# Kernel tuning notes

Measured on AMD Instinct MI355X. Metric: run time of the kernel, lower is better.

Reference implementation:

```python
import jax, jax.numpy as jnp
import numpy as np

N = 100000      # nodes
E = 3200000     # edges
G = 128         # graphs in batch
D_IN = 128
D_H = 256
D_OUT = 64
BN_EPS = 1e-3


def setup_inputs() -> dict:
    key = jax.random.key(0)
    ks = jax.random.split(key, 12)
    h = jax.random.normal(ks[0], (N, D_IN), jnp.float32)
    src = jax.random.randint(ks[1], (E,), 0, N, jnp.int32)
    dst = jax.random.randint(ks[2], (E,), 0, N, jnp.int32)
    graph_ids = jnp.sort(jax.random.randint(ks[3], (N,), 0, G, jnp.int32))
    # GraphConv weights (DGL default: weight + bias)
    W0 = jax.random.normal(ks[4], (D_IN, D_H), jnp.float32) * 0.05
    b0 = jnp.zeros((D_H,), jnp.float32)
    W = jax.random.normal(ks[5], (2, D_H, D_H), jnp.float32) * 0.05  # layers 1,2
    b = jnp.zeros((2, D_H), jnp.float32)
    # BatchNorm1d params (eval mode: running stats), 3 norm layers
    bn_gamma = jnp.ones((3, D_H), jnp.float32)
    bn_beta = jnp.zeros((3, D_H), jnp.float32)
    bn_mean = jax.random.normal(ks[6], (3, D_H), jnp.float32) * 0.1
    bn_var = jax.random.uniform(ks[7], (3, D_H), jnp.float32, 0.5, 1.5)
    # prediction head
    Wp = jax.random.normal(ks[8], (D_H, D_OUT), jnp.float32) * 0.05
    bp = jnp.zeros((D_OUT,), jnp.float32)
    return {"h": h, "W0": W0, "b0": b0, "W": W, "b": b,
            "bn_gamma": bn_gamma, "bn_beta": bn_beta, "bn_mean": bn_mean,
            "bn_var": bn_var, "Wp": Wp, "bp": bp,
            "src": src, "dst": dst, "graph_ids": graph_ids}


def reference(h, W0, b0, W, b, bn_gamma, bn_beta, bn_mean, bn_var, Wp, bp,
              src, dst, graph_ids):
    n = h.shape[0]
    ones_e = jnp.ones(src.shape, h.dtype)
    # symmetric normalization (DGL GraphConv norm='both'), degrees clamped to 1
    out_deg = jax.ops.segment_sum(ones_e, src, num_segments=n)
    in_deg = jax.ops.segment_sum(ones_e, dst, num_segments=n)
    norm_src = jax.lax.rsqrt(jnp.clip(out_deg, 1.0))  # [N]
    norm_dst = jax.lax.rsqrt(jnp.clip(in_deg, 1.0))   # [N]

    def graph_conv(x, Wl, bl):
        x = (x * norm_src[:, None]) @ Wl              # transform first (mult W then aggregate)
        agg = jax.ops.segment_sum(x[src], dst, num_segments=n)  # SpMM: gather+scatter-add
        return agg * norm_dst[:, None] + bl

    Ws = [W0, W[0], W[1]]
    bs = [b0, b[0], b[1]]
    for i in range(3):
        x = h
        h = graph_conv(h, Ws[i], bs[i])
        # BatchNorm1d in eval mode (running stats), eps=1e-3
        h = (h - bn_mean[i]) * jax.lax.rsqrt(bn_var[i] + BN_EPS) * bn_gamma[i] + bn_beta[i]
        h = jax.nn.relu(h) + (x if i != 0 else 0.0)   # residual skipped on first layer

    # mean pooling per graph
    counts = jax.ops.segment_sum(jnp.ones((n,), h.dtype), graph_ids, num_segments=G)
    pooled = jax.ops.segment_sum(h, graph_ids, num_segments=G) / jnp.clip(counts, 1.0)[:, None]
    return pooled @ Wp + bp
```

## Files before the change

### kernel.cpp

```cpp
#include <hip/hip_runtime.h>
#include <hip/hip_bf16.h>

#define NN 100000
#define EE 3200000
#define GG 128
#define D_IN 128
#define D_H 256
#define D_OUT 64
#define BN_EPS 1e-3f
#define PAD 96
#define LDSTRIDE 40
#define X8SCALE 16.0f
#define X8INV   0.0625f

#define NBUCK 782
#define BUCKET_CAP 5120
#define EPT 32

#define GEMM_NWG 6252

typedef __hip_bfloat16 bf16;
typedef __attribute__((ext_vector_type(8))) short short8;
typedef __attribute__((ext_vector_type(4))) float float4v;
typedef __attribute__((ext_vector_type(2))) float float2v;
typedef __attribute__((ext_vector_type(4))) int intv4;
typedef __attribute__((ext_vector_type(4))) unsigned short usv4;

#if __has_builtin(__builtin_amdgcn_cvt_pk_f32_fp8) && __has_builtin(__builtin_amdgcn_cvt_pk_fp8_f32)
#define HAVE_FP8_CVT 1
#endif

__device__ inline float bfbits2f(unsigned short s) {
    union { unsigned int u; float f; } c; c.u = ((unsigned int)s) << 16; return c.f;
}
__device__ inline unsigned short f2bfbits(float f) {
    union { float f; unsigned int u; } c; c.f = f;
    unsigned int r = c.u + 0x7fffu + ((c.u >> 16) & 1u);
    return (unsigned short)(r >> 16);
}
__device__ inline float4 load4us(const unsigned short* p) {
    ushort4 u = *(const ushort4*)p;
    return make_float4(bfbits2f(u.x), bfbits2f(u.y), bfbits2f(u.z), bfbits2f(u.w));
}
__device__ inline void store4us(unsigned short* p, float4 v) {
    ushort4 u;
    u.x = f2bfbits(v.x); u.y = f2bfbits(v.y); u.z = f2bfbits(v.z); u.w = f2bfbits(v.w);
    *(ushort4*)p = u;
}
__device__ inline float4 load4us_nt(const unsigned short* p) {
    usv4 u = __builtin_nontemporal_load((const usv4*)p);
    return make_float4(bfbits2f(u.x), bfbits2f(u.y), bfbits2f(u.z), bfbits2f(u.w));
}

__device__ inline unsigned char enc_fp8(float f) {
#ifdef HAVE_FP8_CVT
    int r = __builtin_amdgcn_cvt_pk_fp8_f32(f, f, 0, false);
    return (unsigned char)(r & 0xFF);
#else
    union { float f; unsigned u; } c; c.f = f;
    unsigned s = (c.u >> 31) << 7;
    float a = fabsf(f);
    if (!(a >= 0.015625f)) {
        int q = (int)rintf(a * 512.0f);
        return (unsigned char)(s | (unsigned)q);
    }
    if (a >= 464.0f) return (unsigned char)(s | 0x7E);
    int e = (int)((c.u >> 23) & 0xFF) - 127;
    int q = (int)rintf(ldexpf(a, 3 - e));
    if (q == 16) { q = 8; e += 1; }
    return (unsigned char)(s | ((unsigned)(e + 7) << 3) | (unsigned)(q - 8));
#endif
}
__device__ inline unsigned int enc4_fp8(float4 v) {
#ifdef HAVE_FP8_CVT
    int r = __builtin_amdgcn_cvt_pk_fp8_f32(v.x, v.y, 0, false);
    r = __builtin_amdgcn_cvt_pk_fp8_f32(v.z, v.w, r, true);
    return (unsigned int)r;
#else
    return (unsigned int)enc_fp8(v.x) | ((unsigned int)enc_fp8(v.y) << 8)
         | ((unsigned int)enc_fp8(v.z) << 16) | ((unsigned int)enc_fp8(v.w) << 24);
#endif
}
__device__ inline float4 dec4_fp8(unsigned int w) {
#ifdef HAVE_FP8_CVT
    float2v lo = __builtin_amdgcn_cvt_pk_f32_fp8((int)w, false);
    float2v hi = __builtin_amdgcn_cvt_pk_f32_fp8((int)w, true);
    return make_float4(lo.x, lo.y, hi.x, hi.y);
#else
    float4 o;
    unsigned b0 = w & 0xFF, b1 = (w >> 8) & 0xFF, b2 = (w >> 16) & 0xFF, b3 = w >> 24;
    auto d1 = [](unsigned b) -> float {
        unsigned s = b >> 7, e = (b >> 3) & 0xF, m = b & 7;
        float v = e ? ldexpf((float)(8 + m), (int)e - 10) : ldexpf((float)m, -9);
        return s ? -v : v;
    };
    o.x = d1(b0); o.y = d1(b1); o.z = d1(b2); o.w = d1(b3);
    return o;
#endif
}

__device__ inline int xcd_swz_gemm(int bid) {
    int x = bid & 7, i = bid >> 3;
    return (x < 4 ? x * 782 : 3128 + (x - 4) * 781) + i;
}

__global__ __launch_bounds__(1024) void k_bucket(const int* __restrict__ src,
                                                 const int* __restrict__ dst,
                                                 int* __restrict__ cursor,
                                                 int* __restrict__ scursor,
                                                 int* __restrict__ ebuf,
                                                 unsigned char* __restrict__ sbuf, int e) {
    __shared__ int hist[NBUCK];
    __shared__ int base[NBUCK];
    __shared__ int shist[NBUCK];
    __shared__ int sbase[NBUCK];
    int t = threadIdx.x;
    for (int i = t; i < NBUCK; i += 1024) { hist[i] = 0; shist[i] = 0; }
    __syncthreads();
    int e0 = blockIdx.x * (1024 * EPT) + t;
    int vals[EPT]; int bks[EPT];
#pragma unroll
    for (int j = 0; j < EPT; ++j) {
        int idx = e0 + j * 1024;
        bks[j] = -1;
        if (idx < e) {
            int s = src[idx], d = dst[idx];
            bks[j] = d >> 7;
            vals[j] = (s << 7) | (d & 127);
            atomicAdd(&hist[bks[j]], 1);
            atomicAdd(&shist[s >> 7], 1);
        }
    }
    __syncthreads();
    for (int i = t; i < NBUCK; i += 1024) {
        int c = hist[i];
        base[i] = c ? atomicAdd(&cursor[i], c) : 0;
        hist[i] = 0;
        int sc = shist[i];
        sbase[i] = sc ? atomicAdd(&scursor[i], sc) : 0;
        shist[i] = 0;
    }
    __syncthreads();
#pragma unroll
    for (int j = 0; j < EPT; ++j) {
        if (bks[j] >= 0) {
            int v = vals[j];
            int rel = base[bks[j]] + atomicAdd(&hist[bks[j]], 1);
            if (rel < BUCKET_CAP) ebuf[bks[j] * BUCKET_CAP + rel] = v;
            int sbk = v >> 14;
            int srel = sbase[sbk] + atomicAdd(&shist[sbk], 1);
            if (srel < BUCKET_CAP) sbuf[(size_t)sbk * BUCKET_CAP + srel] = (unsigned char)((v >> 7) & 127);
        }
    }
}

__global__ __launch_bounds__(256) void k_fill(const int* __restrict__ cursor,
                                              const int* __restrict__ scursor,
                                              const int* __restrict__ ebuf,
                                              const unsigned char* __restrict__ sbuf,
                                              int* __restrict__ col_pad,
                                              int* __restrict__ deg_in,
                                              float* __restrict__ norm_src,
                                              float* __restrict__ norm_dst) {
    __shared__ int lcol[128 * PAD];
    __shared__ int ldeg[128];
    __shared__ int lodeg[128];
    int b = blockIdx.x;
    int t = threadIdx.x;
    if (t < 128) { ldeg[t] = 0; lodeg[t] = 0; }
    __syncthreads();
    int cnt = cursor[b]; if (cnt > BUCKET_CAP) cnt = BUCKET_CAP;
    const int* eb = ebuf + b * BUCKET_CAP;
    for (int i = t; i < cnt; i += 256) {
        int v = eb[i];
        int node = v & 127;
        int s = v >> 7;
        int pos = atomicAdd(&ldeg[node], 1);
        if (pos < PAD) lcol[node * PAD + pos] = s;
    }
    int scnt = scursor[b]; if (scnt > BUCKET_CAP) scnt = BUCKET_CAP;
    const unsigned char* sb = sbuf + (size_t)b * BUCKET_CAP;
    for (int i = t; i < scnt; i += 256) {
        atomicAdd(&lodeg[sb[i]], 1);
    }
    __syncthreads();
    int n0 = b << 7;
    int nn = NN - n0; if (nn > 128) nn = 128;
    int q = (nn * PAD) >> 2;
    int4* gdst = (int4*)(col_pad + (size_t)n0 * PAD);
    const int4* lsrc = (const int4*)lcol;
    for (int i = t; i < q; i += 256) gdst[i] = lsrc[i];
    if (t < nn) {
        int node = n0 + t;
        int din = ldeg[t];
        int dout = lodeg[t];
        deg_in[node] = din;
        norm_dst[node] = rsqrtf((float)(din < 1 ? 1 : din));
        norm_src[node] = rsqrtf((float)(dout < 1 ? 1 : dout));
    }
}

__global__ __launch_bounds__(256) void k_splitw(const float* __restrict__ W0,
                                                const float* __restrict__ Wl,
                                                unsigned short* __restrict__ wsplit) {
    int b = blockIdx.x;
    int n = threadIdx.x;
    const float* Wsrc; unsigned short *hiT, *loT; int K, k;
    if (b < 128)      { k = b;       K = 128; Wsrc = W0;          hiT = wsplit;          loT = wsplit + 32768; }
    else if (b < 384) { k = b - 128; K = 256; Wsrc = Wl;          hiT = wsplit + 65536;  loT = wsplit + 131072; }
    else              { k = b - 384; K = 256; Wsrc = Wl + 65536;  hiT = wsplit + 196608; loT = wsplit + 262144; }
    float w = Wsrc[k * 256 + n];
    unsigned short h = f2bfbits(w);
    hiT[n * K + k] = h;
    loT[n * K + k] = f2bfbits(w - bfbits2f(h));
}

__global__ __launch_bounds__(256) void k_convert(const float* __restrict__ h,
                                                 const float* __restrict__ norm_src,
                                                 unsigned int* __restrict__ xh8, int n) {
    int gid = blockIdx.x * 256 + threadIdx.x;
    int row = gid >> 5;
    int w = gid & 31;
    if (row < n) {
        float s = norm_src[row] * X8SCALE;
        float4 v = *(const float4*)(h + (size_t)row * D_IN + w * 4);
        v.x *= s; v.y *= s; v.z *= s; v.w *= s;
        xh8[(size_t)row * 32 + w] = enc4_fp8(v);
    }
}

__global__ __launch_bounds__(256) void k_spmm0(const unsigned char* __restrict__ x8,
                                               const int* __restrict__ deg_in,
                                               const int* __restrict__ col_pad,
                                               const float* __restrict__ norm_dst,
                                               unsigned short* __restrict__ p, int n) {
    int wv   = threadIdx.x >> 6;
    int lane = threadIdx.x & 63;
    int half = lane >> 5;
    int dl   = lane & 31;
    unsigned lb = (unsigned)dl << 2;
    int r = blockIdx.x * 8 + wv * 2 + half;
    if (r >= n) return;
    int d = deg_in[r]; if (d > PAD) d = PAD;
    int e0 = r * PAD, e1 = e0 + d;
    float ax = 0.f, ay = 0.f, az = 0.f, aw = 0.f;
    int e = e0;
    for (; e + 15 < e1; e += 16) {
        const intv4* cp = (const intv4*)(col_pad + e);
        intv4 i0 = __builtin_nontemporal_load(cp);
        intv4 i1 = __builtin_nontemporal_load(cp + 1);
        intv4 i2 = __builtin_nontemporal_load(cp + 2);
        intv4 i3 = __builtin_nontemporal_load(cp + 3);
        int s[16] = {i0.x, i0.y, i0.z, i0.w, i1.x, i1.y, i1.z, i1.w,
                     i2.x, i2.y, i2.z, i2.w, i3.x, i3.y, i3.z, i3.w};
        unsigned int w[16];
#pragma unroll
        for (int j = 0; j < 16; ++j)
            w[j] = *(const unsigned int*)(x8 + ((((unsigned)s[j]) << 7) | lb));
#pragma unroll
        for (int j = 0; j < 16; ++j) {
            float4 v = dec4_fp8(w[j]);
            ax += v.x; ay += v.y; az += v.z; aw += v.w;
        }
    }
    for (; e + 7 < e1; e += 8) {
        const intv4* cp = (const intv4*)(col_pad + e);
        intv4 i0 = __builtin_nontemporal_load(cp);
        intv4 i1 = __builtin_nontemporal_load(cp + 1);
        int s[8] = {i0.x, i0.y, i0.z, i0.w, i1.x, i1.y, i1.z, i1.w};
        unsigned int w[8];
#pragma unroll
        for (int j = 0; j < 8; ++j)
            w[j] = *(const unsigned int*)(x8 + ((((unsigned)s[j]) << 7) | lb));
#pragma unroll
        for (int j = 0; j < 8; ++j) {
            float4 v = dec4_fp8(w[j]);
            ax += v.x; ay += v.y; az += v.z; aw += v.w;
        }
    }
    for (; e < e1; ++e) {
        float4 v = dec4_fp8(*(const unsigned int*)(x8 + ((((unsigned)col_pad[e]) << 7) | lb)));
        ax += v.x; ay += v.y; az += v.z; aw += v.w;
    }
    float nd = norm_dst[r] * X8INV;
    store4us(p + (size_t)r * D_IN + dl * 4,
             make_float4(ax * nd, ay * nd, az * nd, aw * nd));
}

__global__ __launch_bounds__(256) void k_gemm_bn(const unsigned short* __restrict__ A,
                                                 const unsigned short* __restrict__ WhiT,
                                                 const unsigned short* __restrict__ WloT,
                                                 const float* __restrict__ bias,
                                                 const float* __restrict__ gamma,
                                                 const float* __restrict__ beta,
                                                 const float* __restrict__ mean,
                                                 const float* __restrict__ var,
                                                 unsigned short* __restrict__ H,
                                                 int M, int K) {
    __shared__ __align__(16) unsigned short lds[3 * 64 * LDSTRIDE];
    unsigned short* As = lds;
    unsigned short* Bh = lds + 64 * LDSTRIDE;
    unsigned short* Bl = lds + 2 * 64 * LDSTRIDE;
    int tid = threadIdx.x, wave = tid >> 6, lane = tid & 63, quad = lane >> 4, l15 = lane & 15;
    int sw = xcd_swz_gemm(blockIdx.x);
    int bm0 = (sw >> 2) * 64, bn0 = (sw & 3) * 64;
    int srow = tid >> 2, sseg = tid & 3;
    int agrow = bm0 + srow;
    float4v acc[4];
#pragma unroll
    for (int t = 0; t < 4; ++t) acc[t] = (float4v){0.f, 0.f, 0.f, 0.f};

    for (int k0 = 0; k0 < K; k0 += 32) {
        ushort4 a0 = make_ushort4(0, 0, 0, 0), a1 = a0;
        if (agrow < M) {
            const ushort4* ap = (const ushort4*)(A + (size_t)agrow * K + k0 + sseg * 8);
            a0 = ap[0]; a1 = ap[1];
        }
        ushort4* ad = (ushort4*)&As[srow * LDSTRIDE + sseg * 8];
        ad[0] = a0; ad[1] = a1;
        const ushort4* wh = (const ushort4*)(WhiT + (size_t)(bn0 + srow) * K + k0 + sseg * 8);
        const ushort4* wl = (const ushort4*)(WloT + (size_t)(bn0 + srow) * K + k0 + sseg * 8);
        ushort4* bd = (ushort4*)&Bh[srow * LDSTRIDE + sseg * 8];
        ushort4* ld = (ushort4*)&Bl[srow * LDSTRIDE + sseg * 8];
        bd[0] = wh[0]; bd[1] = wh[1];
        ld[0] = wl[0]; ld[1] = wl[1];
        __syncthreads();
        short8 a = *(const short8*)&As[(wave * 16 + l15) * LDSTRIDE + quad * 8];
#pragma unroll
        for (int nt = 0; nt < 4; ++nt) {
            short8 bh = *(const short8*)&Bh[(nt * 16 + l15) * LDSTRIDE + quad * 8];
            short8 bl = *(const short8*)&Bl[(nt * 16 + l15) * LDSTRIDE + quad * 8];
            acc[nt] = __builtin_amdgcn_mfma_f32_16x16x32_bf16(a, bh, acc[nt], 0, 0, 0);
            acc[nt] = __builtin_amdgcn_mfma_f32_16x16x32_bf16(a, bl, acc[nt], 0, 0, 0);
        }
        __syncthreads();
    }
#pragma unroll
    for (int nt = 0; nt < 4; ++nt) {
        int col = bn0 + nt * 16 + l15;
        float sc = rsqrtf(var[col] + BN_EPS) * gamma[col];
        float off = (bias[col] - mean[col]) * sc + beta[col];
#pragma unroll
        for (int reg = 0; reg < 4; ++reg) {
            int m = bm0 + wave * 16 + quad * 4 + reg;
            if (m < M) {
                float o = fmaxf(acc[nt][reg] * sc + off, 0.f);
                H[(size_t)m * D_H + col] = f2bfbits(o);
            }
        }
    }
}

__global__ __launch_bounds__(256) void k_gemm_x(const unsigned short* __restrict__ A,
                                                const unsigned short* __restrict__ WhiT,
                                                const unsigned short* __restrict__ WloT,
                                                const float* __restrict__ rowscale,
                                                unsigned char* __restrict__ X8,
                                                int M, int K) {
    __shared__ __align__(16) unsigned short lds[3 * 64 * LDSTRIDE];
    unsigned short* As = lds;
    unsigned short* Bh = lds + 64 * LDSTRIDE;
    unsigned short* Bl = lds + 2 * 64 * LDSTRIDE;
    int tid = threadIdx.x, wave = tid >> 6, lane = tid & 63, quad = lane >> 4, l15 = lane & 15;
    int sw = xcd_swz_gemm(blockIdx.x);
    int bm0 = (sw >> 2) * 64, bn0 = (sw & 3) * 64;
    int srow = tid >> 2, sseg = tid & 3;
    int agrow = bm0 + srow;
    float4v acc[4];
#pragma unroll
    for (int t = 0; t < 4; ++t) acc[t] = (float4v){0.f, 0.f, 0.f, 0.f};

    for (int k0 = 0; k0 < K; k0 += 32) {
        ushort4 a0 = make_ushort4(0, 0, 0, 0), a1 = a0;
        if (agrow < M) {
            const ushort4* ap = (const ushort4*)(A + (size_t)agrow * K + k0 + sseg * 8);
            a0 = ap[0]; a1 = ap[1];
        }
        ushort4* ad = (ushort4*)&As[srow * LDSTRIDE + sseg * 8];
        ad[0] = a0; ad[1] = a1;
        const ushort4* wh = (const ushort4*)(WhiT + (size_t)(bn0 + srow) * K + k0 + sseg * 8);
        const ushort4* wl = (const ushort4*)(WloT + (size_t)(bn0 + srow) * K + k0 + sseg * 8);
        ushort4* bd = (ushort4*)&Bh[srow * LDSTRIDE + sseg * 8];
        ushort4* ld = (ushort4*)&Bl[srow * LDSTRIDE + sseg * 8];
        bd[0] = wh[0]; bd[1] = wh[1];
        ld[0] = wl[0]; ld[1] = wl[1];
        __syncthreads();
        short8 a = *(const short8*)&As[(wave * 16 + l15) * LDSTRIDE + quad * 8];
#pragma unroll
        for (int nt = 0; nt < 4; ++nt) {
            short8 bh = *(const short8*)&Bh[(nt * 16 + l15) * LDSTRIDE + quad * 8];
            short8 bl = *(const short8*)&Bl[(nt * 16 + l15) * LDSTRIDE + quad * 8];
            acc[nt] = __builtin_amdgcn_mfma_f32_16x16x32_bf16(a, bh, acc[nt], 0, 0, 0);
            acc[nt] = __builtin_amdgcn_mfma_f32_16x16x32_bf16(a, bl, acc[nt], 0, 0, 0);
        }
        __syncthreads();
    }
#pragma unroll
    for (int reg = 0; reg < 4; ++reg) {
        int m = bm0 + wave * 16 + quad * 4 + reg;
        if (m < M) {
            float s = rowscale[m] * X8SCALE;
#pragma unroll
            for (int nt = 0; nt < 4; ++nt) {
                int col = bn0 + nt * 16 + l15;
                X8[(size_t)m * D_H + col] = enc_fp8(acc[nt][reg] * s);
            }
        }
    }
}

__global__ __launch_bounds__(256) void k_spmm12(const unsigned char* __restrict__ x8,
                                                const int* __restrict__ deg_in,
                                                const int* __restrict__ col_pad,
                                                const float* __restrict__ norm_dst,
                                                const float* __restrict__ bias,
                                                const float* __restrict__ gamma,
                                                const float* __restrict__ beta,
                                                const float* __restrict__ mean,
                                                const float* __restrict__ var,
                                                unsigned short* __restrict__ H, int n) {
    int wv = __builtin_amdgcn_readfirstlane(threadIdx.x >> 6);
    int r = blockIdx.x * 4 + wv;
    if (r >= n) return;
    int lane = threadIdx.x & 63;
    unsigned lb = (unsigned)lane << 2;
    int c = lane * 4;
    int d = deg_in[r]; if (d > PAD) d = PAD;
    int e0 = r * PAD, e1 = e0 + d;
    float ax = 0.f, ay = 0.f, az = 0.f, aw = 0.f;
    int e = e0;
    for (; e + 15 < e1; e += 16) {
        const intv4* cp = (const intv4*)(col_pad + e);
        intv4 i0 = __builtin_nontemporal_load(cp);
        intv4 i1 = __builtin_nontemporal_load(cp + 1);
        intv4 i2 = __builtin_nontemporal_load(cp + 2);
        intv4 i3 = __builtin_nontemporal_load(cp + 3);
        int s[16] = {i0.x, i0.y, i0.z, i0.w, i1.x, i1.y, i1.z, i1.w,
                     i2.x, i2.y, i2.z, i2.w, i3.x, i3.y, i3.z, i3.w};
        unsigned int w[16];
#pragma unroll
        for (int j = 0; j < 16; ++j)
            w[j] = *(const unsigned int*)(x8 + ((((unsigned)s[j]) << 8) | lb));
#pragma unroll
        for (int j = 0; j < 16; ++j) {
            float4 v = dec4_fp8(w[j]);
            ax += v.x; ay += v.y; az += v.z; aw += v.w;
        }
    }
    for (; e + 7 < e1; e += 8) {
        const intv4* cp = (const intv4*)(col_pad + e);
        intv4 i0 = __builtin_nontemporal_load(cp);
        intv4 i1 = __builtin_nontemporal_load(cp + 1);
        int s[8] = {i0.x, i0.y, i0.z, i0.w, i1.x, i1.y, i1.z, i1.w};
        unsigned int w[8];
#pragma unroll
        for (int j = 0; j < 8; ++j)
            w[j] = *(const unsigned int*)(x8 + ((((unsigned)s[j]) << 8) | lb));
#pragma unroll
        for (int j = 0; j < 8; ++j) {
            float4 v = dec4_fp8(w[j]);
            ax += v.x; ay += v.y; az += v.z; aw += v.w;
        }
    }
    for (; e < e1; ++e) {
        float4 v = dec4_fp8(*(const unsigned int*)(x8 + ((((unsigned)col_pad[e]) << 8) | lb)));
        ax += v.x; ay += v.y; az += v.z; aw += v.w;
    }
    float nd = norm_dst[r] * X8INV;
    float4 b4  = *(const float4*)(bias + c);
    float4 g4  = *(const float4*)(gamma + c);
    float4 be4 = *(const float4*)(beta + c);
    float4 m4  = *(const float4*)(mean + c);
    float4 v4  = *(const float4*)(var + c);
    float4 rv = load4us_nt(H + (size_t)r * D_H + c);
    float4 o;
    o.x = fmaxf((ax * nd + b4.x - m4.x) * rsqrtf(v4.x + BN_EPS) * g4.x + be4.x, 0.f) + rv.x;
    o.y = fmaxf((ay * nd + b4.y - m4.y) * rsqrtf(v4.y + BN_EPS) * g4.y + be4.y, 0.f) + rv.y;
    o.z = fmaxf((az * nd + b4.z - m4.z) * rsqrtf(v4.z + BN_EPS) * g4.z + be4.z, 0.f) + rv.z;
    o.w = fmaxf((aw * nd + b4.w - m4.w) * rsqrtf(v4.w + BN_EPS) * g4.w + be4.w, 0.f) + rv.w;
    store4us(H + (size_t)r * D_H + c, o);
}

__global__ __launch_bounds__(256) void k_pool(const unsigned short* __restrict__ h,
                                              const int* __restrict__ gid,
                                              float* __restrict__ pooled,
                                              float* __restrict__ counts, int n) {
    int wave = threadIdx.x >> 6;
    int lane = threadIdx.x & 63;
    int base = blockIdx.x * 256 + wave * 64;
    if (base >= n) return;
    int c = lane * 4;
    int end = base + 64; if (end > n) end = n;
    float ax = 0.f, ay = 0.f, az = 0.f, aw = 0.f;
    int cnt = 0, cur = -1;
    for (int i = base; i < end; ++i) {
        int g = gid[i];
        if (g != cur) {
            if (cnt > 0) {
                atomicAdd(&pooled[cur * D_H + c + 0], ax);
                atomicAdd(&pooled[cur * D_H + c + 1], ay);
                atomicAdd(&pooled[cur * D_H + c + 2], az);
                atomicAdd(&pooled[cur * D_H + c + 3], aw);
                if (lane == 0) atomicAdd(&counts[cur], (float)cnt);
            }
            cur = g; cnt = 0; ax = ay = az = aw = 0.f;
        }
        float4 v = load4us(h + (size_t)i * D_H + c);
        ax += v.x; ay += v.y; az += v.z; aw += v.w;
        cnt++;
    }
    if (cnt > 0) {
        atomicAdd(&pooled[cur * D_H + c + 0], ax);
        atomicAdd(&pooled[cur * D_H + c + 1], ay);
        atomicAdd(&pooled[cur * D_H + c + 2], az);
        atomicAdd(&pooled[cur * D_H + c + 3], aw);
        if (lane == 0) atomicAdd(&counts[cur], (float)cnt);
    }
}

__global__ __launch_bounds__(64) void k_head(const float* __restrict__ pooled,
                                             const float* __restrict__ counts,
                                             const float* __restrict__ Wp,
                                             const float* __restrict__ bp,
                                             float* __restrict__ out) {
    int g = blockIdx.x;
    int t = threadIdx.x;
    __shared__ float p[D_H];
    float inv = 1.0f / fmaxf(counts[g], 1.0f);
    for (int k = t; k < D_H; k += 64) p[k] = pooled[g * D_H + k] * inv;
    __syncthreads();
    float acc = bp[t];
#pragma unroll 8
    for (int k = 0; k < D_H; ++k) acc = fmaf(p[k], Wp[k * D_OUT + t], acc);
    out[g * D_OUT + t] = acc;
}

extern "C" void kernel_launch(void* const* d_in, const int* in_sizes, int n_in,
                              void* d_out, int out_size, void* d_ws, size_t ws_size,
                              hipStream_t stream) {
    (void)in_sizes; (void)n_in; (void)out_size; (void)ws_size;
    const float* h        = (const float*)d_in[0];
    const float* W0       = (const float*)d_in[1];
    const float* b0       = (const float*)d_in[2];
    const float* Wl       = (const float*)d_in[3];
    const float* bl       = (const float*)d_in[4];
    const float* bn_gamma = (const float*)d_in[5];
    const float* bn_beta  = (const float*)d_in[6];
    const float* bn_mean  = (const float*)d_in[7];
    const float* bn_var   = (const float*)d_in[8];
    const float* Wp       = (const float*)d_in[9];
    const float* bp       = (const float*)d_in[10];
    const int*   src      = (const int*)d_in[11];
    const int*   dst      = (const int*)d_in[12];
    const int*   gid      = (const int*)d_in[13];
    float* out = (float*)d_out;

    char* ws = (char*)d_ws;
    size_t off = 0;
    auto alloc = [&](size_t bytes) -> void* {
        void* p = ws + off;
        off += (bytes + 255) & ~(size_t)255;
        return p;
    };
    unsigned int*   bufXh8 = (unsigned int*)alloc((size_t)NN * D_IN);
    unsigned char*  bufX8  = (unsigned char*)alloc((size_t)NN * D_H);
    unsigned short* bufH   = (unsigned short*)alloc((size_t)NN * D_H * 2);
    unsigned short* bufP   = (unsigned short*)alloc((size_t)NN * D_IN * 2);
    int*   col_pad  = (int*)alloc(((size_t)NN * PAD + 64) * 4);
    float* norm_src = (float*)alloc((size_t)NN * 4);
    float* norm_dst = (float*)alloc((size_t)NN * 4);
    int*   degs     = (int*)alloc(((size_t)NN + 2 * NBUCK) * 4);
    int*   deg_in   = degs;
    int*   cursor   = degs + NN;
    int*   scursor  = degs + NN + NBUCK;
    unsigned short* wsplit = (unsigned short*)alloc(327680 * 2);
    float* pooled   = (float*)alloc((size_t)(GG * D_H + GG) * 4);
    float* counts   = pooled + GG * D_H;

    int* ebuf = (int*)bufX8;
    unsigned char* sbuf = (unsigned char*)bufH;

    unsigned short* w0hi = wsplit;
    unsigned short* w0lo = wsplit + 32768;
    unsigned short* w1hi = wsplit + 65536;
    unsigned short* w1lo = wsplit + 131072;
    unsigned short* w2hi = wsplit + 196608;
    unsigned short* w2lo = wsplit + 262144;

    hipMemsetAsync(cursor, 0, (size_t)2 * NBUCK * 4, stream);
    hipMemsetAsync(pooled, 0, (size_t)(GG * D_H + GG) * 4, stream);

    const int NB = (NN + 255) / 256;
    const int SB = (NN + 3) / 4;
    const int SB0 = (NN + 7) / 8;

    k_splitw<<<640, 256, 0, stream>>>(W0, Wl, wsplit);
    k_bucket<<<(EE + 1024 * EPT - 1) / (1024 * EPT), 1024, 0, stream>>>(
        src, dst, cursor, scursor, ebuf, sbuf, EE);
    k_fill<<<NBUCK, 256, 0, stream>>>(cursor, scursor, ebuf, sbuf, col_pad, deg_in,
                                      norm_src, norm_dst);
    k_convert<<<(NN * 32 + 255) / 256, 256, 0, stream>>>(h, norm_src, bufXh8, NN);

    k_spmm0<<<SB0, 256, 0, stream>>>((const unsigned char*)bufXh8, deg_in, col_pad,
                                     norm_dst, bufP, NN);
    k_gemm_bn<<<GEMM_NWG, 256, 0, stream>>>(bufP, w0hi, w0lo, b0,
                                            bn_gamma, bn_beta, bn_mean, bn_var,
                                            bufH, NN, D_IN);
    k_gemm_x<<<GEMM_NWG, 256, 0, stream>>>(bufH, w1hi, w1lo, norm_src, bufX8, NN, D_H);
    k_spmm12<<<SB, 256, 0, stream>>>(bufX8, deg_in, col_pad, norm_dst, bl,
                                     bn_gamma + D_H, bn_beta + D_H,
                                     bn_mean + D_H, bn_var + D_H, bufH, NN);
    k_gemm_x<<<GEMM_NWG, 256, 0, stream>>>(bufH, w2hi, w2lo, norm_src, bufX8, NN, D_H);
    k_spmm12<<<SB, 256, 0, stream>>>(bufX8, deg_in, col_pad, norm_dst, bl + D_H,
                                     bn_gamma + 2 * D_H, bn_beta + 2 * D_H,
                                     bn_mean + 2 * D_H, bn_var + 2 * D_H, bufH, NN);

    k_pool<<<NB, 256, 0, stream>>>(bufH, gid, pooled, counts, NN);
    k_head<<<GG, 64, 0, stream>>>(pooled, counts, Wp, bp, out);
}
```

Measured before the change: 723.7 us.

## Enlarge GEMM tiles to 128x128 with 2x8 MFMA sub-tiles per wave

```diff
diff --git a/kernel.cpp b/kernel.cpp
--- a/kernel.cpp
+++ b/kernel.cpp
@@ -17,7 +17,7 @@
 #define BUCKET_CAP 5120
 #define EPT 32
 
-#define GEMM_NWG 6252
+#define GEMM_NWG 1564
 
 typedef __hip_bfloat16 bf16;
 typedef __attribute__((ext_vector_type(8))) short short8;
@@ -101,7 +101,7 @@
 
 __device__ inline int xcd_swz_gemm(int bid) {
     int x = bid & 7, i = bid >> 3;
-    return (x < 4 ? x * 782 : 3128 + (x - 4) * 781) + i;
+    return (x < 4 ? x * 196 : 784 + (x - 4) * 195) + i;
 }
 
 __global__ __launch_bounds__(1024) void k_bucket(const int* __restrict__ src,
@@ -297,55 +297,63 @@
                                                  const float* __restrict__ var,
                                                  unsigned short* __restrict__ H,
                                                  int M, int K) {
-    __shared__ __align__(16) unsigned short lds[3 * 64 * LDSTRIDE];
+    __shared__ __align__(16) unsigned short lds[3 * 128 * LDSTRIDE];
     unsigned short* As = lds;
-    unsigned short* Bh = lds + 64 * LDSTRIDE;
-    unsigned short* Bl = lds + 2 * 64 * LDSTRIDE;
+    unsigned short* Bh = lds + 128 * LDSTRIDE;
+    unsigned short* Bl = lds + 2 * 128 * LDSTRIDE;
     int tid = threadIdx.x, wave = tid >> 6, lane = tid & 63, quad = lane >> 4, l15 = lane & 15;
     int sw = xcd_swz_gemm(blockIdx.x);
-    int bm0 = (sw >> 2) * 64, bn0 = (sw & 3) * 64;
-    int srow = tid >> 2, sseg = tid & 3;
+    int bm0 = (sw >> 1) * 128, bn0 = (sw & 1) * 128;
+    int srow = tid >> 1, sseg = tid & 1;
     int agrow = bm0 + srow;
-    float4v acc[4];
-#pragma unroll
-    for (int t = 0; t < 4; ++t) acc[t] = (float4v){0.f, 0.f, 0.f, 0.f};
+    float4v acc[2][8];
+#pragma unroll
+    for (int i = 0; i < 2; ++i)
+#pragma unroll
+        for (int j = 0; j < 8; ++j) acc[i][j] = (float4v){0.f, 0.f, 0.f, 0.f};
 
     for (int k0 = 0; k0 < K; k0 += 32) {
-        ushort4 a0 = make_ushort4(0, 0, 0, 0), a1 = a0;
+        ushort4 a0 = make_ushort4(0, 0, 0, 0), a1 = a0, a2 = a0, a3 = a0;
         if (agrow < M) {
-            const ushort4* ap = (const ushort4*)(A + (size_t)agrow * K + k0 + sseg * 8);
-            a0 = ap[0]; a1 = ap[1];
-        }
-        ushort4* ad = (ushort4*)&As[srow * LDSTRIDE + sseg * 8];
-        ad[0] = a0; ad[1] = a1;
-        const ushort4* wh = (const ushort4*)(WhiT + (size_t)(bn0 + srow) * K + k0 + sseg * 8);
-        const ushort4* wl = (const ushort4*)(WloT + (size_t)(bn0 + srow) * K + k0 + sseg * 8);
-        ushort4* bd = (ushort4*)&Bh[srow * LDSTRIDE + sseg * 8];
-        ushort4* ld = (ushort4*)&Bl[srow * LDSTRIDE + sseg * 8];
-        bd[0] = wh[0]; bd[1] = wh[1];
-        ld[0] = wl[0]; ld[1] = wl[1];
+            const ushort4* ap = (const ushort4*)(A + (size_t)agrow * K + k0 + sseg * 16);
+            a0 = ap[0]; a1 = ap[1]; a2 = ap[2]; a3 = ap[3];
+        }
+        ushort4* ad = (ushort4*)&As[srow * LDSTRIDE + sseg * 16];
+        ad[0] = a0; ad[1] = a1; ad[2] = a2; ad[3] = a3;
+        const ushort4* wh = (const ushort4*)(WhiT + (size_t)(bn0 + srow) * K + k0 + sseg * 16);
+        const ushort4* wl = (const ushort4*)(WloT + (size_t)(bn0 + srow) * K + k0 + sseg * 16);
+        ushort4* bd = (ushort4*)&Bh[srow * LDSTRIDE + sseg * 16];
+        ushort4* ld = (ushort4*)&Bl[srow * LDSTRIDE + sseg * 16];
+        bd[0] = wh[0]; bd[1] = wh[1]; bd[2] = wh[2]; bd[3] = wh[3];
+        ld[0] = wl[0]; ld[1] = wl[1]; ld[2] = wl[2]; ld[3] = wl[3];
         __syncthreads();
-        short8 a = *(const short8*)&As[(wave * 16 + l15) * LDSTRIDE + quad * 8];
-#pragma unroll
-        for (int nt = 0; nt < 4; ++nt) {
+        short8 a0f = *(const short8*)&As[(wave * 32 + l15) * LDSTRIDE + quad * 8];
+        short8 a1f = *(const short8*)&As[(wave * 32 + 16 + l15) * LDSTRIDE + quad * 8];
+#pragma unroll
+        for (int nt = 0; nt < 8; ++nt) {
             short8 bh = *(const short8*)&Bh[(nt * 16 + l15) * LDSTRIDE + quad * 8];
             short8 bl = *(const short8*)&Bl[(nt * 16 + l15) * LDSTRIDE + quad * 8];
-            acc[nt] = __builtin_amdgcn_mfma_f32_16x16x32_bf16(a, bh, acc[nt], 0, 0, 0);
-            acc[nt] = __builtin_amdgcn_mfma_f32_16x16x32_bf16(a, bl, acc[nt], 0, 0, 0);
+            acc[0][nt] = __builtin_amdgcn_mfma_f32_16x16x32_bf16(a0f, bh, acc[0][nt], 0, 0, 0);
+            acc[0][nt] = __builtin_amdgcn_mfma_f32_16x16x32_bf16(a0f, bl, acc[0][nt], 0, 0, 0);
+            acc[1][nt] = __builtin_amdgcn_mfma_f32_16x16x32_bf16(a1f, bh, acc[1][nt], 0, 0, 0);
+            acc[1][nt] = __builtin_amdgcn_mfma_f32_16x16x32_bf16(a1f, bl, acc[1][nt], 0, 0, 0);
         }
         __syncthreads();
     }
 #pragma unroll
-    for (int nt = 0; nt < 4; ++nt) {
+    for (int nt = 0; nt < 8; ++nt) {
         int col = bn0 + nt * 16 + l15;
         float sc = rsqrtf(var[col] + BN_EPS) * gamma[col];
         float off = (bias[col] - mean[col]) * sc + beta[col];
 #pragma unroll
-        for (int reg = 0; reg < 4; ++reg) {
-            int m = bm0 + wave * 16 + quad * 4 + reg;
-            if (m < M) {
-                float o = fmaxf(acc[nt][reg] * sc + off, 0.f);
-                H[(size_t)m * D_H + col] = f2bfbits(o);
+        for (int rt = 0; rt < 2; ++rt) {
+#pragma unroll
+            for (int reg = 0; reg < 4; ++reg) {
+                int m = bm0 + wave * 32 + rt * 16 + quad * 4 + reg;
+                if (m < M) {
+                    float o = fmaxf(acc[rt][nt][reg] * sc + off, 0.f);
+                    H[(size_t)m * D_H + col] = f2bfbits(o);
+                }
             }
         }
     }
@@ -357,53 +365,61 @@
                                                 const float* __restrict__ rowscale,
                                                 unsigned char* __restrict__ X8,
                                                 int M, int K) {
-    __shared__ __align__(16) unsigned short lds[3 * 64 * LDSTRIDE];
+    __shared__ __align__(16) unsigned short lds[3 * 128 * LDSTRIDE];
     unsigned short* As = lds;
-    unsigned short* Bh = lds + 64 * LDSTRIDE;
-    unsigned short* Bl = lds + 2 * 64 * LDSTRIDE;
+    unsigned short* Bh = lds + 128 * LDSTRIDE;
+    unsigned short* Bl = lds + 2 * 128 * LDSTRIDE;
     int tid = threadIdx.x, wave = tid >> 6, lane = tid & 63, quad = lane >> 4, l15 = lane & 15;
     int sw = xcd_swz_gemm(blockIdx.x);
-    int bm0 = (sw >> 2) * 64, bn0 = (sw & 3) * 64;
-    int srow = tid >> 2, sseg = tid & 3;
+    int bm0 = (sw >> 1) * 128, bn0 = (sw & 1) * 128;
+    int srow = tid >> 1, sseg = tid & 1;
     int agrow = bm0 + srow;
-    float4v acc[4];
-#pragma unroll
-    for (int t = 0; t < 4; ++t) acc[t] = (float4v){0.f, 0.f, 0.f, 0.f};
+    float4v acc[2][8];
+#pragma unroll
+    for (int i = 0; i < 2; ++i)
+#pragma unroll
+        for (int j = 0; j < 8; ++j) acc[i][j] = (float4v){0.f, 0.f, 0.f, 0.f};
 
     for (int k0 = 0; k0 < K; k0 += 32) {
-        ushort4 a0 = make_ushort4(0, 0, 0, 0), a1 = a0;
+        ushort4 a0 = make_ushort4(0, 0, 0, 0), a1 = a0, a2 = a0, a3 = a0;
         if (agrow < M) {
-            const ushort4* ap = (const ushort4*)(A + (size_t)agrow * K + k0 + sseg * 8);
-            a0 = ap[0]; a1 = ap[1];
-        }
-        ushort4* ad = (ushort4*)&As[srow * LDSTRIDE + sseg * 8];
-        ad[0] = a0; ad[1] = a1;
-        const ushort4* wh = (const ushort4*)(WhiT + (size_t)(bn0 + srow) * K + k0 + sseg * 8);
-        const ushort4* wl = (const ushort4*)(WloT + (size_t)(bn0 + srow) * K + k0 + sseg * 8);
-        ushort4* bd = (ushort4*)&Bh[srow * LDSTRIDE + sseg * 8];
-        ushort4* ld = (ushort4*)&Bl[srow * LDSTRIDE + sseg * 8];
-        bd[0] = wh[0]; bd[1] = wh[1];
-        ld[0] = wl[0]; ld[1] = wl[1];
+            const ushort4* ap = (const ushort4*)(A + (size_t)agrow * K + k0 + sseg * 16);
+            a0 = ap[0]; a1 = ap[1]; a2 = ap[2]; a3 = ap[3];
+        }
+        ushort4* ad = (ushort4*)&As[srow * LDSTRIDE + sseg * 16];
+        ad[0] = a0; ad[1] = a1; ad[2] = a2; ad[3] = a3;
+        const ushort4* wh = (const ushort4*)(WhiT + (size_t)(bn0 + srow) * K + k0 + sseg * 16);
+        const ushort4* wl = (const ushort4*)(WloT + (size_t)(bn0 + srow) * K + k0 + sseg * 16);
+        ushort4* bd = (ushort4*)&Bh[srow * LDSTRIDE + sseg * 16];
+        ushort4* ld = (ushort4*)&Bl[srow * LDSTRIDE + sseg * 16];
+        bd[0] = wh[0]; bd[1] = wh[1]; bd[2] = wh[2]; bd[3] = wh[3];
+        ld[0] = wl[0]; ld[1] = wl[1]; ld[2] = wl[2]; ld[3] = wl[3];
         __syncthreads();
-        short8 a = *(const short8*)&As[(wave * 16 + l15) * LDSTRIDE + quad * 8];
-#pragma unroll
-        for (int nt = 0; nt < 4; ++nt) {
+        short8 a0f = *(const short8*)&As[(wave * 32 + l15) * LDSTRIDE + quad * 8];
+        short8 a1f = *(const short8*)&As[(wave * 32 + 16 + l15) * LDSTRIDE + quad * 8];
+#pragma unroll
+        for (int nt = 0; nt < 8; ++nt) {
             short8 bh = *(const short8*)&Bh[(nt * 16 + l15) * LDSTRIDE + quad * 8];
             short8 bl = *(const short8*)&Bl[(nt * 16 + l15) * LDSTRIDE + quad * 8];
-            acc[nt] = __builtin_amdgcn_mfma_f32_16x16x32_bf16(a, bh, acc[nt], 0, 0, 0);
-            acc[nt] = __builtin_amdgcn_mfma_f32_16x16x32_bf16(a, bl, acc[nt], 0, 0, 0);
+            acc[0][nt] = __builtin_amdgcn_mfma_f32_16x16x32_bf16(a0f, bh, acc[0][nt], 0, 0, 0);
+            acc[0][nt] = __builtin_amdgcn_mfma_f32_16x16x32_bf16(a0f, bl, acc[0][nt], 0, 0, 0);
+            acc[1][nt] = __builtin_amdgcn_mfma_f32_16x16x32_bf16(a1f, bh, acc[1][nt], 0, 0, 0);
+            acc[1][nt] = __builtin_amdgcn_mfma_f32_16x16x32_bf16(a1f, bl, acc[1][nt], 0, 0, 0);
         }
         __syncthreads();
     }
 #pragma unroll
-    for (int reg = 0; reg < 4; ++reg) {
-        int m = bm0 + wave * 16 + quad * 4 + reg;
-        if (m < M) {
-            float s = rowscale[m] * X8SCALE;
-#pragma unroll
-            for (int nt = 0; nt < 4; ++nt) {
-                int col = bn0 + nt * 16 + l15;
-                X8[(size_t)m * D_H + col] = enc_fp8(acc[nt][reg] * s);
+    for (int rt = 0; rt < 2; ++rt) {
+#pragma unroll
+        for (int reg = 0; reg < 4; ++reg) {
+            int m = bm0 + wave * 32 + rt * 16 + quad * 4 + reg;
+            if (m < M) {
+                float s = rowscale[m] * X8SCALE;
+#pragma unroll
+                for (int nt = 0; nt < 8; ++nt) {
+                    int col = bn0 + nt * 16 + l15;
+                    X8[(size_t)m * D_H + col] = enc_fp8(acc[rt][nt][reg] * s);
+                }
             }
         }
     }
```

After: 714.2 us. No clear change (-1.3%).
